# Kernel tuning notes

Measured on AMD Instinct MI355X. Metric: run time of the kernel, lower is better.

## Reference

```python
import jax, jax.numpy as jnp
import numpy as np

N_NODES = 1536
IN_FEATURES = 1433
N_HIDDEN = 64      # total across 8 heads -> 8 per head
N_HEADS = 8
N_CLASSES = 7
NEG_SLOPE = 0.2    # LeakyReLU slope in GATv2 layer


def setup_inputs() -> dict:
    key = jax.random.key(0)
    k_x, k_adj, k_w1, k_a1, k_w2, k_a2 = jax.random.split(key, 6)
    x = jax.random.normal(k_x, (N_NODES, IN_FEATURES), dtype=jnp.float32)
    adj = jax.random.uniform(k_adj, (N_NODES, N_NODES)) < 0.01
    adj = adj | jnp.eye(N_NODES, dtype=bool)
    adj_mat = adj[:, :, None]  # [n, n, 1]
    # layer 1 (share_weights=True -> one linear for l and r), attn vector shared across heads
    s1 = 1.0 / np.sqrt(IN_FEATURES)
    W1 = jax.random.uniform(k_w1, (IN_FEATURES, N_HIDDEN), minval=-s1, maxval=s1, dtype=jnp.float32)
    a1 = jax.random.uniform(k_a1, (N_HIDDEN // N_HEADS,), minval=-1.0, maxval=1.0, dtype=jnp.float32)
    # layer 2: 1 head, n_classes features, is_concat=False (mean over the single head)
    s2 = 1.0 / np.sqrt(N_HIDDEN)
    W2 = jax.random.uniform(k_w2, (N_HIDDEN, N_CLASSES), minval=-s2, maxval=s2, dtype=jnp.float32)
    a2 = jax.random.uniform(k_a2, (N_CLASSES,), minval=-1.0, maxval=1.0, dtype=jnp.float32)
    return {"x": x, "adj_mat": adj_mat, "W1": W1, "a1": a1, "W2": W2, "a2": a2}


def _gatv2_layer(h, adj, W, a, n_heads, is_concat):
    n = h.shape[0]
    g = (h @ W).reshape(n, n_heads, -1)              # shared weights: g_l == g_r == g
    # pairwise scores: e[i,j,h] = a . leaky_relu(g[j] + g[i])  (symmetric since weights shared)
    s = jax.nn.leaky_relu(g[:, None] + g[None, :], NEG_SLOPE)   # [n, n, heads, f]
    e = jnp.einsum('ijhf,f->ijh', s, a)                          # [n, n, heads]
    e = jnp.where(adj, e, -jnp.inf)                              # adj broadcasts [n,n,1]
    att = jax.nn.softmax(e, axis=1)                              # softmax over source nodes j
    out = jnp.einsum('ijh,jhf->ihf', att, g)                     # [n, heads, f]
    if is_concat:
        return out.reshape(n, -1)
    return out.mean(axis=1)


def reference(x, adj_mat, W1, a1, W2, a2):
    # dropout layers are identity in eval mode
    h = _gatv2_layer(x, adj_mat, W1, a1, N_HEADS, True)   # [n, n_hidden]
    h = jax.nn.elu(h)
    return _gatv2_layer(h, adj_mat, W2, a2, 1, False)     # [n, n_classes]
```

## Files before the change

### kernel.cpp

```cpp
#include <hip/hip_runtime.h>

#define N_NODES 1536
#define IN_F    1433
#define HID     64
#define NH      8
#define HF      8
#define NC      7
#define MAXN    64
#define GST     66
#define G1_BLOCKS 384
#define ROWS    4
#define XS_STRIDE 1440

__device__ __forceinline__ float waveAllMax(float v) {
#pragma unroll
    for (int o = 32; o > 0; o >>= 1) v = fmaxf(v, __shfl_xor(v, o, 64));
    return v;
}
__device__ __forceinline__ float waveAllSum(float v) {
#pragma unroll
    for (int o = 32; o > 0; o >>= 1) v += __shfl_xor(v, o, 64);
    return v;
}

__global__ __launch_bounds__(256) void k_front(const float* __restrict__ x,
                                               const float* __restrict__ W1,
                                               const unsigned int* __restrict__ adj,
                                               float* __restrict__ g1,
                                               int* __restrict__ cnt,
                                               int* __restrict__ nbr) {
    __shared__ float xs[ROWS * XS_STRIDE];
    __shared__ float red[4 * 256];
    __shared__ int lc;
    const int t = threadIdx.x;

    if (blockIdx.x < G1_BLOCKS) {
        const int i0 = blockIdx.x * ROWS;
        for (int r = 0; r < ROWS; ++r) {
            const float* xr = x + (size_t)(i0 + r) * IN_F;
            for (int k = t; k < XS_STRIDE; k += 256)
                xs[r * XS_STRIDE + k] = (k < IN_F) ? xr[k] : 0.f;
        }
        __syncthreads();
        const int j = t & 63, q = t >> 6;
        float acc[ROWS] = {0.f, 0.f, 0.f, 0.f};
        const int k0 = q * 360;
        for (int kb = k0; kb < k0 + 360; kb += 4) {
            float w[4];
#pragma unroll
            for (int u = 0; u < 4; ++u) {
                int k = kb + u;
                int kc = (k < IN_F) ? k : (IN_F - 1);
                w[u] = W1[(size_t)kc * HID + j];
            }
#pragma unroll
            for (int r = 0; r < ROWS; ++r) {
                float4 xv = *(const float4*)(xs + r * XS_STRIDE + kb);
                acc[r] += xv.x * w[0] + xv.y * w[1] + xv.z * w[2] + xv.w * w[3];
            }
        }
#pragma unroll
        for (int r = 0; r < ROWS; ++r) red[q * 256 + r * 64 + j] = acc[r];
        __syncthreads();
        float s = red[0 * 256 + t] + red[1 * 256 + t] + red[2 * 256 + t] + red[3 * 256 + t];
        g1[(size_t)(i0 + (t >> 6)) * HID + (t & 63)] = s;
    } else {
        const int i = blockIdx.x - G1_BLOCKS;
        if (t == 0) lc = 0;
        __syncthreads();
        const unsigned int* row = adj + (size_t)i * N_NODES;
        for (int j = t; j < N_NODES; j += 256) {
            if (row[j] != 0u) {
                int p = atomicAdd(&lc, 1);
                if (p < MAXN) nbr[i * MAXN + p] = j;
            }
        }
        __syncthreads();
        if (t == 0) {
            int n = (lc > MAXN) ? MAXN : lc;
            if (n == 0) { nbr[i * MAXN] = i; n = 1; }
            cnt[i] = n;
        }
    }
}

__global__ __launch_bounds__(128) void k_attn1(const float* __restrict__ g1,
                                               const int* __restrict__ cnt,
                                               const int* __restrict__ nbr,
                                               const float* __restrict__ a1,
                                               float* __restrict__ h1) {
    __shared__ float gis[HID];
    __shared__ float gj[MAXN * GST];
    __shared__ float es[NH * GST];
    const int i = blockIdx.x, tid = threadIdx.x;
    const int t = tid & 63, w = tid >> 6;
    const int n = cnt[i];

    if (tid < HID) gis[tid] = g1[(size_t)i * HID + tid];
    const int jn = nbr[i * MAXN + t];

    for (int l0 = 4 * w; l0 < n; l0 += 8) {
        float v[4];
#pragma unroll
        for (int u = 0; u < 4; ++u) {
            int l = l0 + u;
            int lc = (l < n) ? l : (n - 1);
            int j = __shfl(jn, lc, 64);
            v[u] = g1[(size_t)j * HID + t];
        }
#pragma unroll
        for (int u = 0; u < 4; ++u)
            if (l0 + u < n) gj[(l0 + u) * GST + t] = v[u];
    }
    __syncthreads();

    float av[HF];
#pragma unroll
    for (int f = 0; f < HF; ++f) av[f] = a1[f];

    float sc[4];
    if (t < n) {
#pragma unroll
        for (int hh = 0; hh < 4; ++hh) {
            const int h = 4 * w + hh;
            float s = 0.f;
#pragma unroll
            for (int f = 0; f < HF; ++f) {
                float v = gis[h * HF + f] + gj[t * GST + h * HF + f];
                v = (v >= 0.f) ? v : 0.2f * v;
                s += av[f] * v;
            }
            sc[hh] = s;
        }
    } else {
#pragma unroll
        for (int hh = 0; hh < 4; ++hh) sc[hh] = -INFINITY;
    }

#pragma unroll
    for (int hh = 0; hh < 4; ++hh) {
        const int h = 4 * w + hh;
        float m = waveAllMax(sc[hh]);
        float p = (t < n) ? __expf(sc[hh] - m) : 0.f;
        float S = waveAllSum(p);
        es[h * GST + t] = p / S;
    }

    const int c = 32 * w + (t & 31);
    const int h = c >> 3;
    float acc = 0.f;
    for (int l = (t >> 5); l < n; l += 2)
        acc += es[h * GST + l] * gj[l * GST + c];
    acc += __shfl_xor(acc, 32, 64);
    if (t < 32)
        h1[(size_t)i * HID + c] = (acc > 0.f) ? acc : (__expf(acc) - 1.f);
}

__global__ __launch_bounds__(128) void k_back(const float* __restrict__ h1,
                                              const float* __restrict__ W2,
                                              const float* __restrict__ a2,
                                              const int* __restrict__ cnt,
                                              const int* __restrict__ nbr,
                                              float* __restrict__ out) {
    __shared__ float hj[MAXN * GST];
    __shared__ float w2s[HID * NC];
    __shared__ float g2s[MAXN * 8];
    __shared__ float ps[MAXN];
    const int i = blockIdx.x, tid = threadIdx.x;
    const int t = tid & 63, w = tid >> 6;
    const int n = cnt[i];

    for (int k = tid; k < HID * NC; k += 128) w2s[k] = W2[k];
    const int jn = nbr[i * MAXN + t];
    for (int l0 = 4 * w; l0 < n; l0 += 8) {
        float v[4];
#pragma unroll
        for (int u = 0; u < 4; ++u) {
            int l = l0 + u;
            int lc = (l < n) ? l : (n - 1);
            int j = __shfl(jn, lc, 64);
            v[u] = h1[(size_t)j * HID + t];
        }
#pragma unroll
        for (int u = 0; u < 4; ++u)
            if (l0 + u < n) hj[(l0 + u) * GST + t] = v[u];
    }
    __syncthreads();

    if (t < n) {
        const int c0 = 4 * w, c1 = (w == 0) ? 4 : 7;
        for (int c = c0; c < c1; ++c) {
            float s = 0.f;
#pragma unroll
            for (int f = 0; f < HID; ++f)
                s += hj[t * GST + f] * w2s[f * NC + c];
            g2s[t * 8 + c] = s;
        }
    }
    unsigned long long bal = __ballot(t < n && jn == i);
    int ls = (bal != 0ull) ? (__ffsll((long long)bal) - 1) : 0;
    __syncthreads();

    if (w == 0) {
        float scv;
        if (t < n) {
            float s = 0.f;
#pragma unroll
            for (int c = 0; c < NC; ++c) {
                float v = g2s[ls * 8 + c] + g2s[t * 8 + c];
                v = (v >= 0.f) ? v : 0.2f * v;
                s += a2[c] * v;
            }
            scv = s;
        } else scv = -INFINITY;

        float m = waveAllMax(scv);
        float p = (t < n) ? __expf(scv - m) : 0.f;
        ps[t] = p;
        float S = waveAllSum(p);

        if (t < NC) {
            float acc = 0.f;
            for (int l = 0; l < n; ++l)
                acc += ps[l] * g2s[l * 8 + t];
            out[(size_t)i * NC + t] = acc / S;
        }
    }
}

extern "C" void kernel_launch(void* const* d_in, const int* in_sizes, int n_in,
                              void* d_out, int out_size, void* d_ws, size_t ws_size,
                              hipStream_t stream) {
    (void)out_size; (void)ws_size;
    const void* px = nullptr; const void* padj = nullptr;
    const void* pW1 = nullptr; const void* pa1 = nullptr;
    const void* pW2 = nullptr; const void* pa2 = nullptr;
    for (int i = 0; i < n_in; ++i) {
        switch (in_sizes[i]) {
            case N_NODES * IN_F:    px   = d_in[i]; break;
            case N_NODES * N_NODES: padj = d_in[i]; break;
            case IN_F * HID:        pW1  = d_in[i]; break;
            case HF:                pa1  = d_in[i]; break;
            case HID * NC:          pW2  = d_in[i]; break;
            case NC:                pa2  = d_in[i]; break;
            default: break;
        }
    }
    if (!px && n_in > 0)   px   = d_in[0];
    if (!padj && n_in > 1) padj = d_in[1];
    if (!pW1 && n_in > 2)  pW1  = d_in[2];
    if (!pa1 && n_in > 3)  pa1  = d_in[3];
    if (!pW2 && n_in > 4)  pW2  = d_in[4];
    if (!pa2 && n_in > 5)  pa2  = d_in[5];

    char* w = (char*)d_ws;
    size_t off = 0;
    auto carve = [&](size_t bytes) -> char* {
        off = (off + 255) & ~(size_t)255;
        char* p = w + off; off += bytes; return p;
    };
    int*   cnt = (int*)  carve((size_t)N_NODES * 4);
    int*   nbr = (int*)  carve((size_t)N_NODES * MAXN * 4);
    float* g1  = (float*)carve((size_t)N_NODES * HID * 4);
    float* h1  = (float*)carve((size_t)N_NODES * HID * 4);

    float* outp = (float*)d_out;

    k_front<<<G1_BLOCKS + N_NODES, 256, 0, stream>>>((const float*)px, (const float*)pW1,
                                                     (const unsigned int*)padj, g1, cnt, nbr);
    k_attn1<<<N_NODES, 128, 0, stream>>>(g1, cnt, nbr, (const float*)pa1, h1);
    k_back<<<N_NODES, 128, 0, stream>>>(h1, (const float*)pW2, (const float*)pa2,
                                        cnt, nbr, outp);
}
```

Baseline: 115.0 us.

## Fuse layer-2 projection into attention-1 kernel and slim back kernel

The h1·W2 projection now runs at the end of the layer-1 attention kernel, so each node writes an 8-float g2 row instead of a 64-float h1 row. The back kernel becomes one wavefront that gathers compact g2 rows for its neighbours and uses wave reductions for the softmax and the aggregation. This removes the 64-wide neighbour gather and the per-neighbour recompute of the W2 projection in layer 2. The cost is an extra block barrier and a few wave reductions in attn1, which read W2 straight from global memory.

```diff
diff --git a/kernel.cpp b/kernel.cpp
--- a/kernel.cpp
+++ b/kernel.cpp
@@ -88,10 +88,12 @@
                                                const int* __restrict__ cnt,
                                                const int* __restrict__ nbr,
                                                const float* __restrict__ a1,
-                                               float* __restrict__ h1) {
+                                               const float* __restrict__ W2,
+                                               float* __restrict__ g2) {
     __shared__ float gis[HID];
     __shared__ float gj[MAXN * GST];
     __shared__ float es[NH * GST];
+    __shared__ float hrow[HID];
     const int i = blockIdx.x, tid = threadIdx.x;
     const int t = tid & 63, w = tid >> 6;
     const int n = cnt[i];
@@ -152,79 +154,64 @@
     for (int l = (t >> 5); l < n; l += 2)
         acc += es[h * GST + l] * gj[l * GST + c];
     acc += __shfl_xor(acc, 32, 64);
-    if (t < 32)
-        h1[(size_t)i * HID + c] = (acc > 0.f) ? acc : (__expf(acc) - 1.f);
-}
-
-__global__ __launch_bounds__(128) void k_back(const float* __restrict__ h1,
-                                              const float* __restrict__ W2,
-                                              const float* __restrict__ a2,
-                                              const int* __restrict__ cnt,
-                                              const int* __restrict__ nbr,
-                                              float* __restrict__ out) {
-    __shared__ float hj[MAXN * GST];
-    __shared__ float w2s[HID * NC];
+    float hv = (acc > 0.f) ? acc : (__expf(acc) - 1.f);
+    if (t < 32) hrow[c] = hv;
+    __syncthreads();
+
+    const float hvt = hrow[t];
+#pragma unroll
+    for (int cc = 0; cc < 4; ++cc) {
+        const int cG = 4 * w + cc;
+        if (cG < NC) {
+            float v = hvt * W2[t * NC + cG];
+            v = waveAllSum(v);
+            if (t == 0) g2[(size_t)i * 8 + cG] = v;
+        }
+    }
+}
+
+__global__ __launch_bounds__(64) void k_back(const float* __restrict__ g2,
+                                             const float* __restrict__ a2,
+                                             const int* __restrict__ cnt,
+                                             const int* __restrict__ nbr,
+                                             float* __restrict__ out) {
     __shared__ float g2s[MAXN * 8];
-    __shared__ float ps[MAXN];
-    const int i = blockIdx.x, tid = threadIdx.x;
-    const int t = tid & 63, w = tid >> 6;
+    const int i = blockIdx.x, t = threadIdx.x;
     const int n = cnt[i];
-
-    for (int k = tid; k < HID * NC; k += 128) w2s[k] = W2[k];
     const int jn = nbr[i * MAXN + t];
-    for (int l0 = 4 * w; l0 < n; l0 += 8) {
-        float v[4];
-#pragma unroll
-        for (int u = 0; u < 4; ++u) {
-            int l = l0 + u;
-            int lc = (l < n) ? l : (n - 1);
-            int j = __shfl(jn, lc, 64);
-            v[u] = h1[(size_t)j * HID + t];
-        }
-#pragma unroll
-        for (int u = 0; u < 4; ++u)
-            if (l0 + u < n) hj[(l0 + u) * GST + t] = v[u];
-    }
+    const int j = (t < n) ? jn : i;
+
+    float4 lo = *(const float4*)(g2 + (size_t)j * 8);
+    float4 hi = *(const float4*)(g2 + (size_t)j * 8 + 4);
+    float4 slo = *(const float4*)(g2 + (size_t)i * 8);
+    float4 shi = *(const float4*)(g2 + (size_t)i * 8 + 4);
+    *(float4*)(g2s + t * 8) = lo;
+    *(float4*)(g2s + t * 8 + 4) = hi;
     __syncthreads();
 
+    const float self[NC] = {slo.x, slo.y, slo.z, slo.w, shi.x, shi.y, shi.z};
+
+    float scv;
     if (t < n) {
-        const int c0 = 4 * w, c1 = (w == 0) ? 4 : 7;
-        for (int c = c0; c < c1; ++c) {
-            float s = 0.f;
-#pragma unroll
-            for (int f = 0; f < HID; ++f)
-                s += hj[t * GST + f] * w2s[f * NC + c];
-            g2s[t * 8 + c] = s;
-        }
-    }
-    unsigned long long bal = __ballot(t < n && jn == i);
-    int ls = (bal != 0ull) ? (__ffsll((long long)bal) - 1) : 0;
-    __syncthreads();
-
-    if (w == 0) {
-        float scv;
-        if (t < n) {
-            float s = 0.f;
-#pragma unroll
-            for (int c = 0; c < NC; ++c) {
-                float v = g2s[ls * 8 + c] + g2s[t * 8 + c];
-                v = (v >= 0.f) ? v : 0.2f * v;
-                s += a2[c] * v;
-            }
-            scv = s;
-        } else scv = -INFINITY;
-
-        float m = waveAllMax(scv);
-        float p = (t < n) ? __expf(scv - m) : 0.f;
-        ps[t] = p;
-        float S = waveAllSum(p);
-
-        if (t < NC) {
-            float acc = 0.f;
-            for (int l = 0; l < n; ++l)
-                acc += ps[l] * g2s[l * 8 + t];
-            out[(size_t)i * NC + t] = acc / S;
-        }
+        float s = 0.f;
+#pragma unroll
+        for (int c = 0; c < NC; ++c) {
+            float v = self[c] + g2s[t * 8 + c];
+            v = (v >= 0.f) ? v : 0.2f * v;
+            s += a2[c] * v;
+        }
+        scv = s;
+    } else scv = -INFINITY;
+
+    float m = waveAllMax(scv);
+    float p = (t < n) ? __expf(scv - m) : 0.f;
+    float S = waveAllSum(p);
+
+#pragma unroll
+    for (int c = 0; c < NC; ++c) {
+        float v = (t < n) ? p * g2s[t * 8 + c] : 0.f;
+        float s = waveAllSum(v);
+        if (t == c) out[(size_t)i * NC + c] = s / S;
     }
 }
 
@@ -262,13 +249,13 @@
     int*   cnt = (int*)  carve((size_t)N_NODES * 4);
     int*   nbr = (int*)  carve((size_t)N_NODES * MAXN * 4);
     float* g1  = (float*)carve((size_t)N_NODES * HID * 4);
-    float* h1  = (float*)carve((size_t)N_NODES * HID * 4);
+    float* g2  = (float*)carve((size_t)N_NODES * 8 * 4);
 
     float* outp = (float*)d_out;
 
     k_front<<<G1_BLOCKS + N_NODES, 256, 0, stream>>>((const float*)px, (const float*)pW1,
                                                      (const unsigned int*)padj, g1, cnt, nbr);
-    k_attn1<<<N_NODES, 128, 0, stream>>>(g1, cnt, nbr, (const float*)pa1, h1);
-    k_back<<<N_NODES, 128, 0, stream>>>(h1, (const float*)pW2, (const float*)pa2,
-                                        cnt, nbr, outp);
-}
+    k_attn1<<<N_NODES, 128, 0, stream>>>(g1, cnt, nbr, (const float*)pa1,
+                                         (const float*)pW2, g2);
+    k_back<<<N_NODES, 64, 0, stream>>>(g2, (const float*)pa2, cnt, nbr, outp);
+}
```

Result: faster. 110.4 us (-4.0%).
